# Optimization experiments

Hardware: AMD Instinct MI355X
Metric: run time of the kernel (lower is better)

Reference implementation:

```python
import jax, jax.numpy as jnp
import numpy as np

B, DIM, DIMH, DIMC = 1024, 32, 1024, 512
SQRT_HALF_PI = float(np.sqrt(np.pi / 2.0))
SQRT2 = float(np.sqrt(2.0))


def _gsp(x):
    """gaussian_softplus activation from ConditionalICNN."""
    return (SQRT_HALF_PI * x * jax.scipy.special.erf(x / SQRT2)
            + jnp.exp(-0.5 * x * x) + SQRT_HALF_PI * x) / (2.0 * SQRT_HALF_PI)


def setup_inputs() -> dict:
    key = jax.random.key(0)
    _i = [0]
    def nrm(shape, s=0.05):
        _i[0] += 1
        return jax.random.normal(jax.random.fold_in(key, _i[0]), shape, dtype=jnp.float32) * s
    inp = {
        "x": nrm((B, DIM), 1.0),
        "c": nrm((B, DIMC), 1.0),
        # w0 init: log(exp(1)-1) as in DeepConvexFlow
        "w0": jnp.full((1,), float(np.log(np.e - 1.0)), dtype=jnp.float32),
        "w1": jnp.zeros((1,), dtype=jnp.float32),
        "Wz0_w": nrm((DIMH, DIM)), "Wz0_b": nrm((DIMH,)),
        "Wc0_w": nrm((DIMH, DIMC)), "Wc0_b": nrm((DIMH,)),
        "an0_b": nrm((DIMH,)), "an0_logs": nrm((DIMH,), 0.01),
        "Wz1_w": nrm((DIMH, DIMH)), "Wz1_b": nrm((DIMH,)),
        "Wx1_w": nrm((DIMH, DIM)), "Wx1_b": nrm((DIMH,)),
        "Wc1_w": nrm((DIMH, DIMC)), "Wc1_b": nrm((DIMH,)),
        "an1_b": nrm((DIMH,)), "an1_logs": nrm((DIMH,), 0.01),
        "Wz2_w": nrm((DIMH, DIMH)), "Wz2_b": nrm((DIMH,)),
        "Wx2_w": nrm((DIMH, DIM)), "Wx2_b": nrm((DIMH,)),
        "Wc2_w": nrm((DIMH, DIMC)), "Wc2_b": nrm((DIMH,)),
        "an2_b": nrm((DIMH,)), "an2_logs": nrm((DIMH,), 0.01),
        "Wzout_w": nrm((1, DIMH)), "Wxout_w": nrm((1, DIM)), "Wcout_w": nrm((1, DIMC)),
    }
    return inp


def reference(x, c, w0, w1,
              Wz0_w, Wz0_b, Wc0_w, Wc0_b, an0_b, an0_logs,
              Wz1_w, Wz1_b, Wx1_w, Wx1_b, Wc1_w, Wc1_b, an1_b, an1_logs,
              Wz2_w, Wz2_b, Wx2_w, Wx2_b, Wc2_w, Wc2_b, an2_b, an2_logs,
              Wzout_w, Wxout_w, Wcout_w):
    """ConditionalDeepConvexFlow.forward_transform with exact logdet.
    Returns (f = grad_x F(x), logdet = logabsdet of per-sample Hessian)."""

    def pot(x1, c1):  # scalar convex potential F for one sample
        h = Wz0_w @ x1 + Wz0_b + Wc0_w @ c1 + Wc0_b
        z = _gsp((h + an0_b) * jnp.exp(an0_logs))  # ActNormNoLogdet + act
        for (Wz_w, Wz_b, Wx_w, Wx_b, Wc_w, Wc_b, an_b, an_logs) in (
                (Wz1_w, Wz1_b, Wx1_w, Wx1_b, Wc1_w, Wc1_b, an1_b, an1_logs),
                (Wz2_w, Wz2_b, Wx2_w, Wx2_b, Wc2_w, Wc2_b, an2_b, an2_logs)):
            # PosLinear: softplus(W) with gain 1/in_features
            h = (jax.nn.softplus(Wz_w) @ z) / DIMH + Wz_b \
                + Wx_w @ x1 + Wx_b + Wc_w @ c1 + Wc_b
            z = _gsp((h + an_b) * jnp.exp(an_logs))
        icnn = (jax.nn.softplus(Wzout_w) @ z)[0] / DIMH \
               + (Wxout_w @ x1)[0] + (Wcout_w @ c1)[0]
        return jax.nn.softplus(w1)[0] * icnn \
               + jax.nn.softplus(w0)[0] * 0.5 * jnp.sum(x1 * x1)

    f = jax.vmap(jax.grad(pot))(x, c)          # [B, DIM]
    H = jax.vmap(jax.hessian(pot))(x, c)       # [B, DIM, DIM]
    logdet = jnp.linalg.slogdet(H)[1]          # [B]
    return f, logdet
```

## Files before the change

### kernel.cpp

```cpp
#include <hip/hip_runtime.h>

constexpr int NB   = 1024;
constexpr int NDIM = 32;
constexpr int NH   = 1024;
constexpr int NC   = 512;
constexpr int NS   = 8;
constexpr int KSF  = 8;

constexpr float INV_SQRT2PI = 0.3989422804014327f;
constexpr float SQRT_HALF   = 0.70710678118654752f;
constexpr float SQRT_HPI    = 1.2533141373155003f;

typedef __attribute__((ext_vector_type(8))) short short8;
typedef __attribute__((ext_vector_type(4))) short short4v;
typedef __attribute__((ext_vector_type(4))) float float4v;

__device__ __forceinline__ float sp_f(float x) {
  return (x > 20.f) ? x : log1pf(expf(x));
}

__device__ __forceinline__ short f2bf(float f) {
  union { float f; unsigned u; } x; x.f = f;
  const unsigned r = x.u + 0x7fffu + ((x.u >> 16) & 1u);
  return (short)(r >> 16);
}

__device__ __forceinline__ float bf2f(short s) {
  union { unsigned u; float f; } c;
  c.u = ((unsigned)(unsigned short)s) << 16;
  return c.f;
}

__device__ __forceinline__ void async_ld16(const void* g, void* l) {
  __builtin_amdgcn_global_load_lds(
      (const __attribute__((address_space(1))) void*)g,
      (__attribute__((address_space(3))) void*)l, 16, 0, 0);
}

__global__ __launch_bounds__(256) void k_prep(
    const float* __restrict__ Wz1, const float* __restrict__ Wz2,
    const float* __restrict__ Wzout, const float* __restrict__ Wz0,
    const float* __restrict__ Wx1, const float* __restrict__ Wx2,
    const float* __restrict__ Wc0, const float* __restrict__ Wc1,
    const float* __restrict__ Wc2, const float* __restrict__ Cc,
    short* __restrict__ S1b, short* __restrict__ S1Tb,
    short* __restrict__ S2b, short* __restrict__ S2Tb,
    short* __restrict__ Wc0b, short* __restrict__ Wc1b, short* __restrict__ Wc2b,
    short* __restrict__ Ccb, short* __restrict__ W0Tb,
    short* __restrict__ Wx1Tb, short* __restrict__ Wx2Tb,
    float* __restrict__ so)
{
  const int idx = blockIdx.x * 256 + threadIdx.x;
  const int i = idx >> 10, p = idx & 1023;
  const float v1 = sp_f(Wz1[idx]);
  const short b1 = f2bf(v1);
  S1b[idx] = b1; S1Tb[p * NH + i] = b1;
  const float v2 = sp_f(Wz2[idx]);
  const short b2 = f2bf(v2);
  S2b[idx] = b2; S2Tb[p * NH + i] = b2;
  if (idx < NH) so[idx] = sp_f(Wzout[idx]);
  if (idx < NH * NC) {
    Wc0b[idx] = f2bf(Wc0[idx]);
    Wc1b[idx] = f2bf(Wc1[idx]);
    Wc2b[idx] = f2bf(Wc2[idx]);
  }
  if (idx < NB * NC) Ccb[idx] = f2bf(Cc[idx]);
  if (idx < NDIM * NH) {
    const int j = idx >> 10, pp = idx & 1023;
    W0Tb[idx]  = f2bf(Wz0[pp * NDIM + j]);
    Wx1Tb[idx] = f2bf(Wx1[pp * NDIM + j]);
    Wx2Tb[idx] = f2bf(Wx2[pp * NDIM + j]);
  }
}

template<int EPI>
__global__ __launch_bounds__(256) void k_gemm(
    const float* __restrict__ A, const float* __restrict__ Bt,
    float* __restrict__ C, int K, int lda, float scale)
{
  __shared__ float As[16][68];
  __shared__ float Bs[16][68];
  const int tid  = threadIdx.y * 16 + threadIdx.x;
  const int arow = tid >> 2;
  const int acol = (tid & 3) << 2;
  const int m0 = blockIdx.y << 6;
  const int n0 = blockIdx.x << 6;

  float acc[4][4];
#pragma unroll
  for (int i = 0; i < 4; ++i)
#pragma unroll
    for (int j = 0; j < 4; ++j) acc[i][j] = 0.f;

  const int R = m0 + arow;
  for (int k0 = 0; k0 < K; k0 += 16) {
    const float4 av = *reinterpret_cast<const float4*>(&A[(size_t)R * lda + k0 + acol]);
    As[acol + 0][arow] = av.x; As[acol + 1][arow] = av.y;
    As[acol + 2][arow] = av.z; As[acol + 3][arow] = av.w;
    const float4 bv = *reinterpret_cast<const float4*>(&Bt[(size_t)(n0 + arow) * K + k0 + acol]);
    Bs[acol + 0][arow] = bv.x; Bs[acol + 1][arow] = bv.y;
    Bs[acol + 2][arow] = bv.z; Bs[acol + 3][arow] = bv.w;
    __syncthreads();
#pragma unroll
    for (int kk = 0; kk < 16; ++kk) {
      const float4 a  = *reinterpret_cast<const float4*>(&As[kk][threadIdx.y << 2]);
      const float4 bb = *reinterpret_cast<const float4*>(&Bs[kk][threadIdx.x << 2]);
      const float am[4] = {a.x, a.y, a.z, a.w};
      const float bn[4] = {bb.x, bb.y, bb.z, bb.w};
#pragma unroll
      for (int i2 = 0; i2 < 4; ++i2)
#pragma unroll
        for (int j2 = 0; j2 < 4; ++j2)
          acc[i2][j2] = fmaf(am[i2], bn[j2], acc[i2][j2]);
    }
    __syncthreads();
  }
#pragma unroll
  for (int i2 = 0; i2 < 4; ++i2) {
    const int row = m0 + (threadIdx.y << 2) + i2;
    const int col = n0 + (threadIdx.x << 2);
    float* cp = &C[(size_t)row * NH + col];
    float4 o;
    o.x = acc[i2][0] * scale; o.y = acc[i2][1] * scale;
    o.z = acc[i2][2] * scale; o.w = acc[i2][3] * scale;
    if constexpr (EPI == 1) {
      const float4 cur = *reinterpret_cast<const float4*>(cp);
      o.x += cur.x; o.y += cur.y; o.z += cur.z; o.w += cur.w;
    }
    *reinterpret_cast<float4*>(cp) = o;
  }
}

__global__ __launch_bounds__(256) void k_m128(
    const short* __restrict__ A, const short* __restrict__ Bt,
    float* __restrict__ C, float scale, int K, int ldc)
{
  __shared__ short As[128 * 32];
  __shared__ short Bs[128 * 32];
  const int tid  = threadIdx.x;
  const int wave = tid >> 6, lane = tid & 63;
  const int m0 = blockIdx.x << 7, n0 = blockIdx.y << 7;
  const int wm = (wave >> 1) << 6, wn = (wave & 1) << 6;
  const int qd = lane >> 4, md = lane & 15;
  const int sr = lane >> 2;
  const int sc = (lane & 3) << 3;

  float4v acc[4][4];
#pragma unroll
  for (int i = 0; i < 4; ++i)
#pragma unroll
    for (int j = 0; j < 4; ++j) acc[i][j] = (float4v)(0.f);

  for (int k0 = 0; k0 < K; k0 += 32) {
#pragma unroll
    for (int i = 0; i < 2; ++i) {
      const int ch  = wave * 2 + i;
      const int row = ch * 16 + sr;
      async_ld16(&A [(size_t)(m0 + row) * K + k0 + sc], &As[ch * 512]);
      async_ld16(&Bt[(size_t)(n0 + row) * K + k0 + sc], &Bs[ch * 512]);
    }
    __syncthreads();
    short8 af[4], bfr[4];
#pragma unroll
    for (int t = 0; t < 4; ++t) {
      af[t]  = *(const short8*)&As[(wm + t * 16 + md) * 32 + qd * 8];
      bfr[t] = *(const short8*)&Bs[(wn + t * 16 + md) * 32 + qd * 8];
    }
#pragma unroll
    for (int i = 0; i < 4; ++i)
#pragma unroll
      for (int j = 0; j < 4; ++j)
        acc[i][j] = __builtin_amdgcn_mfma_f32_16x16x32_bf16(bfr[j], af[i], acc[i][j], 0, 0, 0);
    __syncthreads();
  }

#pragma unroll
  for (int i = 0; i < 4; ++i) {
    const int rowg = m0 + wm + i * 16 + md;
#pragma unroll
    for (int j = 0; j < 4; ++j) {
      const int colb = n0 + wn + j * 16 + (qd << 2);
      float4 o;
      o.x = acc[i][j][0] * scale; o.y = acc[i][j][1] * scale;
      o.z = acc[i][j][2] * scale; o.w = acc[i][j][3] * scale;
      *reinterpret_cast<float4*>(&C[(size_t)rowg * ldc + colb]) = o;
    }
  }
}

template<int EPI>
__global__ __launch_bounds__(256) void k_mgemm(
    const short* __restrict__ A, const short* __restrict__ Bt,
    short* __restrict__ o1, short* __restrict__ o2,
    const float* __restrict__ gvec, const float* __restrict__ dvec,
    const short* __restrict__ wepiT,
    float scale, int K, int b0)
{
  __shared__ short As[128 * 32];
  __shared__ short Bs[128 * 32];
  const int tid  = threadIdx.x;
  const int wave = tid >> 6, lane = tid & 63;
  const int m0 = blockIdx.x << 7, n0 = blockIdx.y << 7;
  const int wm = (wave >> 1) << 6, wn = (wave & 1) << 6;
  const int qd = lane >> 4, md = lane & 15;

  float4v acc[4][4];
#pragma unroll
  for (int i = 0; i < 4; ++i)
#pragma unroll
    for (int j = 0; j < 4; ++j) acc[i][j] = (float4v)(0.f);

  const int sr = lane >> 2;
  const int sc = (lane & 3) << 3;

  for (int k0 = 0; k0 < K; k0 += 32) {
#pragma unroll
    for (int i = 0; i < 2; ++i) {
      const int ch  = wave * 2 + i;
      const int row = ch * 16 + sr;
      async_ld16(&A [(size_t)(m0 + row) * K + k0 + sc], &As[ch * 512]);
      async_ld16(&Bt[(size_t)(n0 + row) * K + k0 + sc], &Bs[ch * 512]);
    }
    __syncthreads();
    short8 af[4], bfr[4];
#pragma unroll
    for (int t = 0; t < 4; ++t) {
      af[t]  = *(const short8*)&As[(wm + t * 16 + md) * 32 + qd * 8];
      bfr[t] = *(const short8*)&Bs[(wn + t * 16 + md) * 32 + qd * 8];
    }
#pragma unroll
    for (int i = 0; i < 4; ++i)
#pragma unroll
      for (int j = 0; j < 4; ++j)
        acc[i][j] = __builtin_amdgcn_mfma_f32_16x16x32_bf16(bfr[j], af[i], acc[i][j], 0, 0, 0);
    __syncthreads();
  }

#pragma unroll
  for (int i = 0; i < 4; ++i) {
    const int rowg = m0 + wm + i * 16 + md;
    const int b = b0 + (rowg >> 5);
    const int j2 = rowg & 31;
    const size_t bNH = (size_t)b * NH;
#pragma unroll
    for (int j = 0; j < 4; ++j) {
      const int colb = n0 + wn + j * 16 + (qd << 2);
      const float4 dq = *(const float4*)&dvec[bNH + colb];
      const short4v wq = *(const short4v*)&wepiT[(size_t)j2 * NH + colb];
      const float dqv[4] = {dq.x, dq.y, dq.z, dq.w};
      float v[4];
      short4v o1v;
#pragma unroll
      for (int r = 0; r < 4; ++r) {
        v[r] = acc[i][j][r] * scale + bf2f(wq[r]);
        o1v[r] = f2bf(v[r] * dqv[r]);
      }
      *(short4v*)&o1[(size_t)rowg * NH + colb] = o1v;
      if constexpr (EPI == 2) {
        const float4 gg = *(const float4*)&gvec[bNH + colb];
        const float ggv[4] = {gg.x, gg.y, gg.z, gg.w};
        short4v o2v;
#pragma unroll
        for (int r = 0; r < 4; ++r) o2v[r] = f2bf(v[r] * ggv[r]);
        *(short4v*)&o2[(size_t)rowg * NH + colb] = o2v;
      }
    }
  }
}

__global__ __launch_bounds__(256) void k_mgemm64(
    const short* __restrict__ A, const short* __restrict__ Bt,
    float* __restrict__ C, float scale, int K)
{
  __shared__ short As[64 * 32];
  __shared__ short Bs[64 * 32];
  const int tid  = threadIdx.x;
  const int wave = tid >> 6, lane = tid & 63;
  const int m0 = blockIdx.x << 6, n0 = blockIdx.y << 6;
  const int wm = (wave >> 1) << 5, wn = (wave & 1) << 5;
  const int qd = lane >> 4, md = lane & 15;
  const int sr = lane >> 2;
  const int sc = (lane & 3) << 3;

  float4v acc[2][2];
#pragma unroll
  for (int i = 0; i < 2; ++i)
#pragma unroll
    for (int j = 0; j < 2; ++j) acc[i][j] = (float4v)(0.f);

  for (int k0 = 0; k0 < K; k0 += 32) {
    const int row = wave * 16 + sr;
    async_ld16(&A [(size_t)(m0 + row) * K + k0 + sc], &As[wave * 512]);
    async_ld16(&Bt[(size_t)(n0 + row) * K + k0 + sc], &Bs[wave * 512]);
    __syncthreads();
    short8 af[2], bfr[2];
#pragma unroll
    for (int t = 0; t < 2; ++t) {
      af[t]  = *(const short8*)&As[(wm + t * 16 + md) * 32 + qd * 8];
      bfr[t] = *(const short8*)&Bs[(wn + t * 16 + md) * 32 + qd * 8];
    }
#pragma unroll
    for (int i = 0; i < 2; ++i)
#pragma unroll
      for (int j = 0; j < 2; ++j)
        acc[i][j] = __builtin_amdgcn_mfma_f32_16x16x32_bf16(bfr[j], af[i], acc[i][j], 0, 0, 0);
    __syncthreads();
  }

#pragma unroll
  for (int i = 0; i < 2; ++i) {
    const int rowg = m0 + wm + i * 16 + md;
#pragma unroll
    for (int j = 0; j < 2; ++j) {
      const int colb = n0 + wn + j * 16 + (qd << 2);
      float4 o;
      o.x = acc[i][j][0] * scale; o.y = acc[i][j][1] * scale;
      o.z = acc[i][j][2] * scale; o.w = acc[i][j][3] * scale;
      *reinterpret_cast<float4*>(&C[(size_t)rowg * NH + colb]) = o;
    }
  }
}

__global__ __launch_bounds__(256) void k_act(
    const float* __restrict__ HP, const float* __restrict__ HPC_l,
    const float* __restrict__ bA, const float* __restrict__ bB,
    const float* __restrict__ bC,
    const float* __restrict__ anb, const float* __restrict__ anl,
    short* __restrict__ Zbf, float* __restrict__ G, float* __restrict__ U,
    int hasC)
{
  const int idx = blockIdx.x * 256 + threadIdx.x;
  const int i = idx & 1023;
  float bias = bA[i] + bB[i] + anb[i];
  if (hasC) bias += bC[i];
  const float el = expf(anl[i]);
  const float hc = HPC_l[(size_t)(idx >> 10) * (3 * NH) + i];
  const float a = (HP[idx] + hc + bias) * el;
  const float pdf = expf(-0.5f * a * a);
  const float er = erff(a * SQRT_HALF);
  Zbf[idx] = f2bf((SQRT_HPI * a * er + pdf + SQRT_HPI * a) * INV_SQRT2PI);
  G[idx] = 0.5f * (1.f + er) * el;
  U[idx] = pdf * INV_SQRT2PI * el * el;
}

__global__ __launch_bounds__(256) void k_act2(
    const float* __restrict__ HP, const float* __restrict__ HPC_l,
    const float* __restrict__ bA, const float* __restrict__ bB,
    const float* __restrict__ bC,
    const float* __restrict__ anb, const float* __restrict__ anl,
    const float* __restrict__ so,
    float* __restrict__ SD2, short* __restrict__ D2gbf)
{
  const int idx = blockIdx.x * 256 + threadIdx.x;
  const int i = idx & 1023;
  const float bias = bA[i] + bB[i] + bC[i] + anb[i];
  const float el = expf(anl[i]);
  const float hc = HPC_l[(size_t)(idx >> 10) * (3 * NH) + i];
  const float a = (HP[idx] + hc + bias) * el;
  const float pdf = expf(-0.5f * a * a);
  const float er = erff(a * SQRT_HALF);
  const float g = 0.5f * (1.f + er) * el;
  const float u = pdf * INV_SQRT2PI * el * el;
  const float t2 = so[i] * (1.f / NH);
  SD2[idx] = sqrtf(fmaxf(t2 * u, 0.f));
  D2gbf[idx] = f2bf(t2 * g);
}

__global__ __launch_bounds__(256) void k_bw1(
    const float* __restrict__ T1, const float* __restrict__ G1,
    const float* __restrict__ U1,
    short* __restrict__ E1bf, float* __restrict__ SD1)
{
  const int idx = blockIdx.x * 256 + threadIdx.x;
  const float t = T1[idx];
  E1bf[idx] = f2bf(t * G1[idx]);
  SD1[idx] = sqrtf(fmaxf(t * U1[idx], 0.f));
}

__global__ __launch_bounds__(256) void k_bw0(
    const float* __restrict__ T0, const float* __restrict__ U0,
    const float* __restrict__ G0,
    float* __restrict__ D0, short* __restrict__ GT0b)
{
  const int idx = blockIdx.x * 256 + threadIdx.x;
  const float t = T0[idx];
  D0[idx] = t * U0[idx];
  GT0b[idx] = f2bf(t * G0[idx]);
}

__global__ __launch_bounds__(256) void k_scale0(
    const float* __restrict__ G0, const float* __restrict__ Wz0,
    short* __restrict__ Ah1, int b0)
{
  const int idx = blockIdx.x * 256 + threadIdx.x;
  const int p = idx & 1023, r = idx >> 10;
  const int b = b0 + (r >> 5), j = r & 31;
  Ah1[idx] = f2bf(G0[(size_t)b * NH + p] * Wz0[p * NDIM + j]);
}

__global__ __launch_bounds__(256) void k_fgemm(
    const short* __restrict__ A0, const short* __restrict__ A1,
    const short* __restrict__ A2,
    const short* __restrict__ W0T, const short* __restrict__ W1T,
    const short* __restrict__ W2T,
    float* __restrict__ partF)
{
  const int mb = blockIdx.x;
  const int ks = blockIdx.y;
  const int term = blockIdx.z;
  const short* A  = (term == 0) ? A0 : (term == 1) ? A1 : A2;
  const short* WT = (term == 0) ? W0T : (term == 1) ? W1T : W2T;
  const int wave = threadIdx.x >> 6, lane = threadIdx.x & 63;
  const int qd = lane >> 4, md = lane & 15;
  const int m0 = mb * 128 + wave * 32;
  const int kbeg = ks * (NH / KSF);

  float4v acc[2][2];
#pragma unroll
  for (int i = 0; i < 2; ++i)
#pragma unroll
    for (int j = 0; j < 2; ++j) acc[i][j] = (float4v)(0.f);

  for (int k0 = kbeg; k0 < kbeg + NH / KSF; k0 += 32) {
    const int kk = k0 + qd * 8;
    short8 af[2], bfr[2];
    af[0]  = *(const short8*)&A[(size_t)(m0 + md) * NH + kk];
    af[1]  = *(const short8*)&A[(size_t)(m0 + 16 + md) * NH + kk];
    bfr[0] = *(const short8*)&WT[(size_t)md * NH + kk];
    bfr[1] = *(const short8*)&WT[(size_t)(16 + md) * NH + kk];
#pragma unroll
    for (int i = 0; i < 2; ++i)
#pragma unroll
      for (int j = 0; j < 2; ++j)
        acc[i][j] = __builtin_amdgcn_mfma_f32_16x16x32_bf16(af[i], bfr[j], acc[i][j], 0, 0, 0);
  }

  float* out = &partF[(size_t)(term * KSF + ks) * NB * 32];
#pragma unroll
  for (int i = 0; i < 2; ++i)
#pragma unroll
    for (int j = 0; j < 2; ++j)
#pragma unroll
      for (int r = 0; r < 4; ++r) {
        const int row = m0 + i * 16 + qd * 4 + r;
        const int col = j * 16 + md;
        out[(size_t)row * 32 + col] = acc[i][j][r];
      }
}

__global__ __launch_bounds__(256) void k_fred(
    const float* __restrict__ partF, const float* __restrict__ X,
    const float* __restrict__ Wxout,
    const float* __restrict__ w0p, const float* __restrict__ w1p,
    float* __restrict__ outF)
{
  const int e = blockIdx.x * 256 + threadIdx.x;
  float s = 0.f;
#pragma unroll
  for (int p = 0; p < 3 * KSF; ++p) s += partF[(size_t)p * NB * 32 + e];
  const float spw0 = sp_f(w0p[0]);
  const float spw1 = sp_f(w1p[0]);
  outF[e] = spw1 * (s + Wxout[e & 31]) + spw0 * X[e];
}

__global__ __launch_bounds__(256) void k_gram(
    const short* __restrict__ Q1, const short* __restrict__ Q2,
    const short* __restrict__ W0T, const float* __restrict__ D0,
    float* __restrict__ partH, int b0)
{
  const int ns = blockIdx.x, bl = blockIdx.y;
  const int b = b0 + bl;
  const int wave = threadIdx.x >> 6, lane = threadIdx.x & 63;
  const int wm = (wave >> 1) << 4, wn = (wave & 1) << 4;
  const int qd = lane >> 4, md = lane & 15;
  const int kbeg = ns << 7;
  const size_t rb = (size_t)bl * 32 * NH;

  float4v acc = (float4v)(0.f);

  for (int k0 = kbeg; k0 < kbeg + 128; k0 += 32) {
    const int kk = k0 + qd * 8;
    const short8 ar = *(const short8*)&W0T[(size_t)(wm + md) * NH + kk];
    float dd[8];
    *(float4*)&dd[0] = *(const float4*)&D0[(size_t)b * NH + kk];
    *(float4*)&dd[4] = *(const float4*)&D0[(size_t)b * NH + kk + 4];
    short8 af;
#pragma unroll
    for (int e = 0; e < 8; ++e) af[e] = f2bf(bf2f(ar[e]) * dd[e]);
    const short8 bfr = *(const short8*)&W0T[(size_t)(wn + md) * NH + kk];
    acc = __builtin_amdgcn_mfma_f32_16x16x32_bf16(af, bfr, acc, 0, 0, 0);
  }
#pragma unroll
  for (int l = 0; l < 2; ++l) {
    const short* Q = (l == 0) ? Q1 : Q2;
    for (int k0 = kbeg; k0 < kbeg + 128; k0 += 32) {
      const int kk = k0 + qd * 8;
      const short8 af  = *(const short8*)&Q[rb + (size_t)(wm + md) * NH + kk];
      const short8 bfr = *(const short8*)&Q[rb + (size_t)(wn + md) * NH + kk];
      acc = __builtin_amdgcn_mfma_f32_16x16x32_bf16(af, bfr, acc, 0, 0, 0);
    }
  }

  float* out = &partH[((size_t)bl * NS + ns) * 1024];
#pragma unroll
  for (int r = 0; r < 4; ++r)
    out[(wm + qd * 4 + r) * 32 + (wn + md)] = acc[r];
}

__global__ __launch_bounds__(256) void k_gram2(
    const float* __restrict__ partH,
    const float* __restrict__ w0p, const float* __restrict__ w1p,
    float* __restrict__ outLD, int b0)
{
  const int bl = blockIdx.x, b = b0 + bl, tid = threadIdx.x;
  __shared__ float sH[32][33];
  __shared__ float sred[32];
  const float spw0 = sp_f(w0p[0]);
  const float spw1 = sp_f(w1p[0]);
  const float* base = &partH[(size_t)bl * NS * 1024];
#pragma unroll
  for (int r = 0; r < 4; ++r) {
    const int e = r * 256 + tid;
    float s = 0.f;
#pragma unroll
    for (int ns = 0; ns < NS; ++ns) s += base[ns * 1024 + e];
    float h = s * spw1;
    const int row = e >> 5, col = e & 31;
    if (row == col) h += spw0;
    sH[row][col] = h;
  }
  __syncthreads();

  float ldacc = 0.f;
  for (int c = 0; c < 32; ++c) {
    if (tid >= c && tid < 32) {
      float s = sH[tid][c];
      for (int m = 0; m < c; ++m) s -= sH[tid][m] * sH[c][m];
      sred[tid] = s;
    }
    __syncthreads();
    const float sc = sred[c];
    if (tid >= c && tid < 32) {
      const float lcc = sqrtf(sc);
      sH[tid][c] = (tid == c) ? lcc : sred[tid] / lcc;
    }
    ldacc += logf(sc);
    __syncthreads();
  }
  if (tid == 0) outLD[b] = ldacc;
}

extern "C" void kernel_launch(void* const* d_in, const int* in_sizes, int n_in,
                              void* d_out, int out_size, void* d_ws, size_t ws_size,
                              hipStream_t stream)
{
  const float* X    = (const float*)d_in[0];
  const float* Cc   = (const float*)d_in[1];
  const float* w0   = (const float*)d_in[2];
  const float* w1   = (const float*)d_in[3];
  const float* Wz0w = (const float*)d_in[4];
  const float* Wz0b = (const float*)d_in[5];
  const float* Wc0w = (const float*)d_in[6];
  const float* Wc0b = (const float*)d_in[7];
  const float* an0b = (const float*)d_in[8];
  const float* an0l = (const float*)d_in[9];
  const float* Wz1w = (const float*)d_in[10];
  const float* Wz1b = (const float*)d_in[11];
  const float* Wx1w = (const float*)d_in[12];
  const float* Wx1b = (const float*)d_in[13];
  const float* Wc1w = (const float*)d_in[14];
  const float* Wc1b = (const float*)d_in[15];
  const float* an1b = (const float*)d_in[16];
  const float* an1l = (const float*)d_in[17];
  const float* Wz2w = (const float*)d_in[18];
  const float* Wz2b = (const float*)d_in[19];
  const float* Wx2w = (const float*)d_in[20];
  const float* Wx2b = (const float*)d_in[21];
  const float* Wc2w = (const float*)d_in[22];
  const float* Wc2b = (const float*)d_in[23];
  const float* an2b = (const float*)d_in[24];
  const float* an2l = (const float*)d_in[25];
  const float* Wzoutw = (const float*)d_in[26];
  const float* Wxoutw = (const float*)d_in[27];

  float* ws = (float*)d_ws;
  size_t off = 0;
  auto alloc = [&](size_t n) {
    float* p = ws + off; off += (n + 3) & ~(size_t)3; return p;
  };
  const size_t HH = (size_t)NH * NH;
  const size_t BH = (size_t)NB * NH;

  short* S1b  = (short*)alloc(HH / 2);
  short* S2b  = (short*)alloc(HH / 2);
  short* S1Tb = (short*)alloc(HH / 2);
  short* S2Tb = (short*)alloc(HH / 2);
  short* Wc0bb = (short*)alloc((size_t)NH * NC / 2);
  short* Wc1bb = (short*)alloc((size_t)NH * NC / 2);
  short* Wc2bb = (short*)alloc((size_t)NH * NC / 2);
  short* Ccb  = (short*)alloc((size_t)NB * NC / 2);
  short* W0Tb = (short*)alloc((size_t)NDIM * NH / 2);
  short* Wx1Tb = (short*)alloc((size_t)NDIM * NH / 2);
  short* Wx2Tb = (short*)alloc((size_t)NDIM * NH / 2);
  float* so   = alloc(NH);
  float* HP   = alloc(BH);
  float* HPC  = alloc((size_t)NB * 3 * NH);
  short* Z0b  = (short*)alloc(BH / 2);
  short* Z1b  = (short*)alloc(BH / 2);
  float* G0   = alloc(BH);
  float* U0   = alloc(BH);
  float* G1   = alloc(BH);
  float* U1   = alloc(BH);
  float* SD2  = alloc(BH);
  short* D2gb = (short*)alloc(BH / 2);
  float* T1   = alloc(BH);
  short* E1b  = (short*)alloc(BH / 2);
  float* SD1  = alloc(BH);
  float* T0   = alloc(BH);
  float* D0   = alloc(BH);
  short* GT0b = (short*)alloc(BH / 2);
  float* partF = alloc((size_t)3 * KSF * NB * 32);

  const size_t avail_f = ws_size / sizeof(float);
  int CB = 32;
  const int cands[6] = {1024, 512, 256, 128, 64, 32};
  for (int ci = 0; ci < 6; ++ci) {
    const size_t need = off + 4 * ((size_t)cands[ci] * 32 * NH / 2 + 4)
                      + (size_t)cands[ci] * NS * 1024 + 64;
    if (need <= avail_f) { CB = cands[ci]; break; }
  }
  const size_t chunk_sh = (size_t)CB * 32 * NH;
  short* Ah1 = (short*)alloc(chunk_sh / 2);
  short* A2b = (short*)alloc(chunk_sh / 2);
  short* Q1b = (short*)alloc(chunk_sh / 2);
  short* Q2b = (short*)alloc(chunk_sh / 2);
  float* partH = alloc((size_t)CB * NS * 1024);

  float* outF  = (float*)d_out;
  float* outLD = (float*)d_out + NB * NDIM;

  const dim3 blk2(16, 16);
  const dim3 gridX(16, NB / 64);
  const dim3 gridE(NB * NH / 256);
  const dim3 grid64(NB / 64, NH / 64);
  const dim3 gridC(NB / 128, 3 * NH / 128);
  const float invH = 1.0f / (float)NH;

  k_prep<<<dim3(HH / 256), dim3(256), 0, stream>>>(
      Wz1w, Wz2w, Wzoutw, Wz0w, Wx1w, Wx2w, Wc0w, Wc1w, Wc2w, Cc,
      S1b, S1Tb, S2b, S2Tb, Wc0bb, Wc1bb, Wc2bb, Ccb, W0Tb, Wx1Tb, Wx2Tb, so);

  k_m128<<<gridC, dim3(256), 0, stream>>>(Ccb, Wc0bb, HPC, 1.f, NC, 3 * NH);

  k_gemm<0><<<gridX, blk2, 0, stream>>>(X, Wz0w, HP, NDIM, NDIM, 1.f);
  k_act<<<gridE, dim3(256), 0, stream>>>(HP, HPC + 0 * NH, Wz0b, Wc0b, nullptr,
                                         an0b, an0l, Z0b, G0, U0, 0);
  k_mgemm64<<<grid64, dim3(256), 0, stream>>>(Z0b, S1b, HP, invH, NH);
  k_gemm<1><<<gridX, blk2, 0, stream>>>(X, Wx1w, HP, NDIM, NDIM, 1.f);
  k_act<<<gridE, dim3(256), 0, stream>>>(HP, HPC + 1 * NH, Wz1b, Wx1b, Wc1b,
                                         an1b, an1l, Z1b, G1, U1, 1);
  k_mgemm64<<<grid64, dim3(256), 0, stream>>>(Z1b, S2b, HP, invH, NH);
  k_gemm<1><<<gridX, blk2, 0, stream>>>(X, Wx2w, HP, NDIM, NDIM, 1.f);
  k_act2<<<gridE, dim3(256), 0, stream>>>(HP, HPC + 2 * NH, Wz2b, Wx2b, Wc2b,
                                          an2b, an2l, so, SD2, D2gb);
  k_mgemm64<<<grid64, dim3(256), 0, stream>>>(D2gb, S2Tb, T1, invH, NH);
  k_bw1<<<gridE, dim3(256), 0, stream>>>(T1, G1, U1, E1b, SD1);
  k_mgemm64<<<grid64, dim3(256), 0, stream>>>(E1b, S1Tb, T0, invH, NH);
  k_bw0<<<gridE, dim3(256), 0, stream>>>(T0, U0, G0, D0, GT0b);

  k_fgemm<<<dim3(8, KSF, 3), dim3(256), 0, stream>>>(
      GT0b, E1b, D2gb, W0Tb, Wx1Tb, Wx2Tb, partF);
  k_fred<<<dim3(NB * 32 / 256), dim3(256), 0, stream>>>(
      partF, X, Wxoutw, w0, w1, outF);

  const dim3 gridJ(CB * 32 / 128, NH / 128);
  const dim3 gridS((size_t)CB * 32 * NH / 256);
  const dim3 gridG(NS, CB);
  for (int b0 = 0; b0 < NB; b0 += CB) {
    k_scale0<<<gridS, dim3(256), 0, stream>>>(G0, Wz0w, Ah1, b0);
    k_mgemm<2><<<gridJ, dim3(256), 0, stream>>>(Ah1, S1b, Q1b, A2b,
                                                G1, SD1, Wx1Tb, invH, NH, b0);
    k_mgemm<1><<<gridJ, dim3(256), 0, stream>>>(A2b, S2b, Q2b, nullptr,
                                                nullptr, SD2, Wx2Tb, invH, NH, b0);
    k_gram<<<gridG, dim3(256), 0, stream>>>(Q1b, Q2b, W0Tb, D0, partH, b0);
    k_gram2<<<dim3(CB), dim3(256), 0, stream>>>(partH, w0, w1, outLD, b0);
  }
}
```

Before: 756.1 us.

## Fuse backward elementwise epilogues into GEMMs and hoist per-sample epilogue loads

The two backward elementwise kernels (k_bw1, k_bw0) are folded into the epilogue of k_mgemm64, so the T1/T0 intermediates are no longer written and re-read. The X-projection GEMMs now accumulate straight into the precomputed conditioning buffer, which removes the separate HP write for layer 0. In k_mgemm the per-sample dvec/gvec loads are hoisted out of the inner loop. Q2b now reuses the Ah1 buffer, which shrinks the workspace and can allow a larger chunk size CB. The cost is extra epilogue work and register pressure in the GEMMs.

```diff
diff --git a/kernel.cpp b/kernel.cpp
--- a/kernel.cpp
+++ b/kernel.cpp
@@ -76,7 +76,7 @@
 template<int EPI>
 __global__ __launch_bounds__(256) void k_gemm(
     const float* __restrict__ A, const float* __restrict__ Bt,
-    float* __restrict__ C, int K, int lda, float scale)
+    float* __restrict__ C, int K, int lda, int ldc)
 {
   __shared__ float As[16][68];
   __shared__ float Bs[16][68];
@@ -119,10 +119,9 @@
   for (int i2 = 0; i2 < 4; ++i2) {
     const int row = m0 + (threadIdx.y << 2) + i2;
     const int col = n0 + (threadIdx.x << 2);
-    float* cp = &C[(size_t)row * NH + col];
+    float* cp = &C[(size_t)row * ldc + col];
     float4 o;
-    o.x = acc[i2][0] * scale; o.y = acc[i2][1] * scale;
-    o.z = acc[i2][2] * scale; o.w = acc[i2][3] * scale;
+    o.x = acc[i2][0]; o.y = acc[i2][1]; o.z = acc[i2][2]; o.w = acc[i2][3];
     if constexpr (EPI == 1) {
       const float4 cur = *reinterpret_cast<const float4*>(cp);
       o.x += cur.x; o.y += cur.y; o.z += cur.z; o.w += cur.w;
@@ -236,17 +235,24 @@
     __syncthreads();
   }
 
-#pragma unroll
-  for (int i = 0; i < 4; ++i) {
-    const int rowg = m0 + wm + i * 16 + md;
-    const int b = b0 + (rowg >> 5);
-    const int j2 = rowg & 31;
-    const size_t bNH = (size_t)b * NH;
-#pragma unroll
-    for (int j = 0; j < 4; ++j) {
-      const int colb = n0 + wn + j * 16 + (qd << 2);
-      const float4 dq = *(const float4*)&dvec[bNH + colb];
+  const int bbase = b0 + ((m0 + wm) >> 5);
+  const size_t bNH0 = (size_t)bbase * NH, bNH1 = bNH0 + NH;
+#pragma unroll
+  for (int j = 0; j < 4; ++j) {
+    const int colb = n0 + wn + j * 16 + (qd << 2);
+    const float4 dqA = *(const float4*)&dvec[bNH0 + colb];
+    const float4 dqB = *(const float4*)&dvec[bNH1 + colb];
+    float4 ggA, ggB;
+    if constexpr (EPI == 2) {
+      ggA = *(const float4*)&gvec[bNH0 + colb];
+      ggB = *(const float4*)&gvec[bNH1 + colb];
+    }
+#pragma unroll
+    for (int i = 0; i < 4; ++i) {
+      const int rowg = m0 + wm + i * 16 + md;
+      const int j2 = rowg & 31;
       const short4v wq = *(const short4v*)&wepiT[(size_t)j2 * NH + colb];
+      const float4 dq = (i < 2) ? dqA : dqB;
       const float dqv[4] = {dq.x, dq.y, dq.z, dq.w};
       float v[4];
       short4v o1v;
@@ -257,7 +263,7 @@
       }
       *(short4v*)&o1[(size_t)rowg * NH + colb] = o1v;
       if constexpr (EPI == 2) {
-        const float4 gg = *(const float4*)&gvec[bNH + colb];
+        const float4 gg = (i < 2) ? ggA : ggB;
         const float ggv[4] = {gg.x, gg.y, gg.z, gg.w};
         short4v o2v;
 #pragma unroll
@@ -268,9 +274,13 @@
   }
 }
 
+template<int FEPI>
 __global__ __launch_bounds__(256) void k_mgemm64(
     const short* __restrict__ A, const short* __restrict__ Bt,
-    float* __restrict__ C, float scale, int K)
+    float* __restrict__ C,
+    const float* __restrict__ auxA, const float* __restrict__ auxB,
+    short* __restrict__ ob, float* __restrict__ of1,
+    float scale)
 {
   __shared__ short As[64 * 32];
   __shared__ short Bs[64 * 32];
@@ -288,10 +298,10 @@
 #pragma unroll
     for (int j = 0; j < 2; ++j) acc[i][j] = (float4v)(0.f);
 
-  for (int k0 = 0; k0 < K; k0 += 32) {
+  for (int k0 = 0; k0 < NH; k0 += 32) {
     const int row = wave * 16 + sr;
-    async_ld16(&A [(size_t)(m0 + row) * K + k0 + sc], &As[wave * 512]);
-    async_ld16(&Bt[(size_t)(n0 + row) * K + k0 + sc], &Bs[wave * 512]);
+    async_ld16(&A [(size_t)(m0 + row) * NH + k0 + sc], &As[wave * 512]);
+    async_ld16(&Bt[(size_t)(n0 + row) * NH + k0 + sc], &Bs[wave * 512]);
     __syncthreads();
     short8 af[2], bfr[2];
 #pragma unroll
@@ -313,10 +323,30 @@
 #pragma unroll
     for (int j = 0; j < 2; ++j) {
       const int colb = n0 + wn + j * 16 + (qd << 2);
-      float4 o;
-      o.x = acc[i][j][0] * scale; o.y = acc[i][j][1] * scale;
-      o.z = acc[i][j][2] * scale; o.w = acc[i][j][3] * scale;
-      *reinterpret_cast<float4*>(&C[(size_t)rowg * NH + colb]) = o;
+      const size_t oi = (size_t)rowg * NH + colb;
+      if constexpr (FEPI == 0) {
+        float4 o;
+        o.x = acc[i][j][0] * scale; o.y = acc[i][j][1] * scale;
+        o.z = acc[i][j][2] * scale; o.w = acc[i][j][3] * scale;
+        *reinterpret_cast<float4*>(&C[oi]) = o;
+      } else {
+        const float4 g4 = *(const float4*)&auxA[oi];
+        const float4 u4 = *(const float4*)&auxB[oi];
+        const float gv[4] = {g4.x, g4.y, g4.z, g4.w};
+        const float uv[4] = {u4.x, u4.y, u4.z, u4.w};
+        short4v eb;
+        float sd[4];
+#pragma unroll
+        for (int r = 0; r < 4; ++r) {
+          const float t = acc[i][j][r] * scale;
+          eb[r] = f2bf(t * gv[r]);
+          if constexpr (FEPI == 3) sd[r] = sqrtf(fmaxf(t * uv[r], 0.f));
+          else                     sd[r] = t * uv[r];
+        }
+        *(short4v*)&ob[oi] = eb;
+        float4 s4; s4.x = sd[0]; s4.y = sd[1]; s4.z = sd[2]; s4.w = sd[3];
+        *(float4*)&of1[oi] = s4;
+      }
     }
   }
 }
@@ -335,7 +365,8 @@
   if (hasC) bias += bC[i];
   const float el = expf(anl[i]);
   const float hc = HPC_l[(size_t)(idx >> 10) * (3 * NH) + i];
-  const float a = (HP[idx] + hc + bias) * el;
+  const float hp = HP ? HP[idx] : 0.f;
+  const float a = (hp + hc + bias) * el;
   const float pdf = expf(-0.5f * a * a);
   const float er = erff(a * SQRT_HALF);
   Zbf[idx] = f2bf((SQRT_HPI * a * er + pdf + SQRT_HPI * a) * INV_SQRT2PI);
@@ -364,28 +395,6 @@
   const float t2 = so[i] * (1.f / NH);
   SD2[idx] = sqrtf(fmaxf(t2 * u, 0.f));
   D2gbf[idx] = f2bf(t2 * g);
-}
-
-__global__ __launch_bounds__(256) void k_bw1(
-    const float* __restrict__ T1, const float* __restrict__ G1,
-    const float* __restrict__ U1,
-    short* __restrict__ E1bf, float* __restrict__ SD1)
-{
-  const int idx = blockIdx.x * 256 + threadIdx.x;
-  const float t = T1[idx];
-  E1bf[idx] = f2bf(t * G1[idx]);
-  SD1[idx] = sqrtf(fmaxf(t * U1[idx], 0.f));
-}
-
-__global__ __launch_bounds__(256) void k_bw0(
-    const float* __restrict__ T0, const float* __restrict__ U0,
-    const float* __restrict__ G0,
-    float* __restrict__ D0, short* __restrict__ GT0b)
-{
-  const int idx = blockIdx.x * 256 + threadIdx.x;
-  const float t = T0[idx];
-  D0[idx] = t * U0[idx];
-  GT0b[idx] = f2bf(t * G0[idx]);
 }
 
 __global__ __launch_bounds__(256) void k_scale0(
@@ -613,10 +622,8 @@
   float* U1   = alloc(BH);
   float* SD2  = alloc(BH);
   short* D2gb = (short*)alloc(BH / 2);
-  float* T1   = alloc(BH);
   short* E1b  = (short*)alloc(BH / 2);
   float* SD1  = alloc(BH);
-  float* T0   = alloc(BH);
   float* D0   = alloc(BH);
   short* GT0b = (short*)alloc(BH / 2);
   float* partF = alloc((size_t)3 * KSF * NB * 32);
@@ -625,7 +632,7 @@
   int CB = 32;
   const int cands[6] = {1024, 512, 256, 128, 64, 32};
   for (int ci = 0; ci < 6; ++ci) {
-    const size_t need = off + 4 * ((size_t)cands[ci] * 32 * NH / 2 + 4)
+    const size_t need = off + 3 * ((size_t)cands[ci] * 32 * NH / 2 + 4)
                       + (size_t)cands[ci] * NS * 1024 + 64;
     if (need <= avail_f) { CB = cands[ci]; break; }
   }
@@ -633,7 +640,7 @@
   short* Ah1 = (short*)alloc(chunk_sh / 2);
   short* A2b = (short*)alloc(chunk_sh / 2);
   short* Q1b = (short*)alloc(chunk_sh / 2);
-  short* Q2b = (short*)alloc(chunk_sh / 2);
+  short* Q2b = Ah1;
   float* partH = alloc((size_t)CB * NS * 1024);
 
   float* outF  = (float*)d_out;
@@ -651,22 +658,24 @@
       S1b, S1Tb, S2b, S2Tb, Wc0bb, Wc1bb, Wc2bb, Ccb, W0Tb, Wx1Tb, Wx2Tb, so);
 
   k_m128<<<gridC, dim3(256), 0, stream>>>(Ccb, Wc0bb, HPC, 1.f, NC, 3 * NH);
-
-  k_gemm<0><<<gridX, blk2, 0, stream>>>(X, Wz0w, HP, NDIM, NDIM, 1.f);
-  k_act<<<gridE, dim3(256), 0, stream>>>(HP, HPC + 0 * NH, Wz0b, Wc0b, nullptr,
+  k_gemm<1><<<gridX, blk2, 0, stream>>>(X, Wz0w, HPC + 0 * NH, NDIM, NDIM, 3 * NH);
+  k_gemm<1><<<gridX, blk2, 0, stream>>>(X, Wx1w, HPC + 1 * NH, NDIM, NDIM, 3 * NH);
+  k_gemm<1><<<gridX, blk2, 0, stream>>>(X, Wx2w, HPC + 2 * NH, NDIM, NDIM, 3 * NH);
+
+  k_act<<<gridE, dim3(256), 0, stream>>>(nullptr, HPC + 0 * NH, Wz0b, Wc0b, nullptr,
                                          an0b, an0l, Z0b, G0, U0, 0);
-  k_mgemm64<<<grid64, dim3(256), 0, stream>>>(Z0b, S1b, HP, invH, NH);
-  k_gemm<1><<<gridX, blk2, 0, stream>>>(X, Wx1w, HP, NDIM, NDIM, 1.f);
+  k_mgemm64<0><<<grid64, dim3(256), 0, stream>>>(Z0b, S1b, HP, nullptr, nullptr,
+                                                 nullptr, nullptr, invH);
   k_act<<<gridE, dim3(256), 0, stream>>>(HP, HPC + 1 * NH, Wz1b, Wx1b, Wc1b,
                                          an1b, an1l, Z1b, G1, U1, 1);
-  k_mgemm64<<<grid64, dim3(256), 0, stream>>>(Z1b, S2b, HP, invH, NH);
-  k_gemm<1><<<gridX, blk2, 0, stream>>>(X, Wx2w, HP, NDIM, NDIM, 1.f);
+  k_mgemm64<0><<<grid64, dim3(256), 0, stream>>>(Z1b, S2b, HP, nullptr, nullptr,
+                                                 nullptr, nullptr, invH);
   k_act2<<<gridE, dim3(256), 0, stream>>>(HP, HPC + 2 * NH, Wz2b, Wx2b, Wc2b,
                                           an2b, an2l, so, SD2, D2gb);
-  k_mgemm64<<<grid64, dim3(256), 0, stream>>>(D2gb, S2Tb, T1, invH, NH);
-  k_bw1<<<gridE, dim3(256), 0, stream>>>(T1, G1, U1, E1b, SD1);
-  k_mgemm64<<<grid64, dim3(256), 0, stream>>>(E1b, S1Tb, T0, invH, NH);
-  k_bw0<<<gridE, dim3(256), 0, stream>>>(T0, U0, G0, D0, GT0b);
+  k_mgemm64<3><<<grid64, dim3(256), 0, stream>>>(D2gb, S2Tb, nullptr, G1, U1,
+                                                 E1b, SD1, invH);
+  k_mgemm64<4><<<grid64, dim3(256), 0, stream>>>(E1b, S1Tb, nullptr, G0, U0,
+                                                 GT0b, D0, invH);
 
   k_fgemm<<<dim3(8, KSF, 3), dim3(256), 0, stream>>>(
       GT0b, E1b, D2gb, W0Tb, Wx1Tb, Wx2Tb, partF);
```

New measurement: 743.6 us. Within noise of the previous version (-1.7%).
